# Kernel tuning notes

Hardware: AMD Instinct MI355X
Metric: run time of the kernel (lower is better)

The kernel has to match this reference:

```python
import jax, jax.numpy as jnp
import numpy as np

ETA = 1e-5
MIN_SIGMA = 1e-6

def setup_inputs() -> dict:
    key = jax.random.key(0)
    k1, k2, k3, k4 = jax.random.split(key, 4)
    B, N0, N1, D = 32, 1024, 1024, 128
    xt = jax.random.normal(k1, (B, D), dtype=jnp.float32)
    t = jax.random.uniform(k2, (B,), dtype=jnp.float32)
    x0_ref = jax.random.normal(k3, (N0, D), dtype=jnp.float32)
    x1_ref = jax.random.normal(k4, (N1, D), dtype=jnp.float32)
    sigma_w = jnp.zeros((1,), dtype=jnp.float32)  # learned scalar of the sigma_model
    return {"xt": xt, "t": t, "x0_ref": x0_ref, "x1_ref": x1_ref, "sigma_w": sigma_w}


def reference(xt, t, x0_ref, x1_ref, sigma_w):
    # Equivalent to ExplicitFlowMatcher.compute_explicit_flow_vcond (implementation='vcond',
    # use_full_gaussian_prefactor=True). The chunked online-softmax loop computes exactly a
    # softmax over all (N0,N1) pairs; here we express it with GEMMs instead of materializing
    # the [B,N0,N1,D] conditional-flow tensor (v_cond is affine in x0, x1, xt so the weighted
    # sum decomposes into matmuls).
    B, D = xt.shape
    Df = jnp.asarray(D, xt.dtype)

    # pairwise squared distances ||x1_j - x0_i||^2 via norms + GEMM  -> [N0,N1]
    x0n = jnp.sum(x0_ref * x0_ref, axis=-1)            # [N0]
    x1n = jnp.sum(x1_ref * x1_ref, axis=-1)            # [N1]
    dot01 = x0_ref @ x1_ref.T                          # [N0,N1]
    dist01 = x0n[:, None] + x1n[None, :] - 2.0 * dot01  # [N0,N1]

    # sigma_model: softplus(w)*||x1-x0||/sqrt(D) + min_sigma, then bridge scale in t
    sigma_space = jax.nn.softplus(sigma_w[0]) * jnp.sqrt(jnp.maximum(dist01, 0.0) / Df) + MIN_SIGMA
    bridge = jnp.sqrt((t + ETA) * (1.0 - t + ETA))     # [B]
    sigma_t = sigma_space[None, :, :] * bridge[:, None, None]  # [B,N0,N1]

    # ||xt_b - mu_t(i,j)||^2 with mu_t = (1-t)x0 + t x1, expanded into GEMM terms
    tb = t[:, None, None]
    omt = 1.0 - tb
    xtn = jnp.sum(xt * xt, axis=-1)                    # [B]
    xt_x0 = xt @ x0_ref.T                              # [B,N0]
    xt_x1 = xt @ x1_ref.T                              # [B,N1]
    mu_norm2 = (omt * omt) * x0n[None, :, None] + (tb * tb) * x1n[None, None, :] \
               + (2.0 * tb * omt) * dot01[None, :, :]
    xt_mu = omt * xt_x0[:, :, None] + tb * xt_x1[:, None, :]
    dist2 = xtn[:, None, None] - 2.0 * xt_mu + mu_norm2  # [B,N0,N1]

    # Gaussian log-weight with full prefactor
    logw = -dist2 / (2.0 * sigma_t * sigma_t) - Df * jnp.log(sigma_t)  # [B,N0,N1]

    # stable softmax over the (N0,N1) pairs (== the online max/den/num recursion)
    m = jnp.max(logw, axis=(1, 2), keepdims=True)
    w = jnp.exp(logw - m)                               # [B,N0,N1]
    den = jnp.sum(w, axis=(1, 2))                       # [B]

    # v_cond = x1 - x0 + c_t*(xt - mu_t) = c_t*xt + a*x0 + b*x1 (affine in x0,x1)
    c_t = (1.0 - 2.0 * t) / (2.0 * (t + ETA) * (1.0 - t + ETA))  # [B]
    a = -1.0 - c_t * (1.0 - t)
    b = 1.0 - c_t * t
    wx0 = jnp.einsum('bij,id->bd', w, x0_ref)
    wx1 = jnp.einsum('bij,jd->bd', w, x1_ref)

    den_c = jnp.maximum(den, 1e-12)[:, None]
    num = c_t[:, None] * xt * den[:, None] + a[:, None] * wx0 + b[:, None] * wx1
    return num / den_c
```

## Files before the change

kernel.cpp:

```cpp
#include <hip/hip_runtime.h>
#include <math.h>

#define ETA 1e-5f
#define MIN_SIGMA 1e-6f

constexpr int NN = 1024;
constexpr int ND = 128;

constexpr size_t OFF_MAXKEY = 0;
constexpr size_t OFF_DEN    = 32;
constexpr size_t OFF_RW     = 64;
constexpr size_t OFF_CW     = OFF_RW + 32 * 1024;
constexpr size_t OFF_X0N    = OFF_CW + 32 * 1024;
constexpr size_t OFF_X1N    = OFF_X0N + 1024;
constexpr size_t OFF_AP     = OFF_X1N + 1024;
constexpr size_t OFF_BP     = OFF_AP + 32 * 1024;
constexpr size_t OFF_C2     = OFF_BP + 32 * 1024;
constexpr size_t OFF_DOT    = ((OFF_C2 + 32 + 63) / 64) * 64;

__device__ __forceinline__ unsigned fkey(float x) {
  unsigned u = __float_as_uint(x);
  return (u & 0x80000000u) ? ~u : (u | 0x80000000u);
}
__device__ __forceinline__ float funkey(unsigned u) {
  return (u & 0x80000000u) ? __uint_as_float(u & 0x7fffffffu)
                           : __uint_as_float(~u);
}

__global__ __launch_bounds__(256) void k_ab(const float* __restrict__ xt,
                                            const float* __restrict__ tarr,
                                            const float* __restrict__ x0,
                                            const float* __restrict__ x1,
                                            float* __restrict__ ws) {
  __shared__ __align__(16) float xts[ND];
  int b = blockIdx.x >> 2, q = blockIdx.x & 3;
  int tid = threadIdx.x;
  if (tid < ND) xts[tid] = xt[(size_t)b * ND + tid];
  __syncthreads();

  float tb = tarr[b];
  float omt = 1.f - tb;
  float ib2 = 1.f / ((tb + ETA) * (1.f - tb + ETA));

  float xtn = 0.f;
#pragma unroll
  for (int k4 = 0; k4 < ND / 4; k4++) {
    float4 xv = *(const float4*)&xts[k4 * 4];
    xtn += xv.x * xv.x + xv.y * xv.y + xv.z * xv.z + xv.w * xv.w;
  }

  int i = q * 256 + tid;
  float acc0 = 0.f, acc1 = 0.f, n0 = 0.f, n1 = 0.f;
#pragma unroll 8
  for (int k4 = 0; k4 < ND / 4; k4++) {
    float4 xv = *(const float4*)&xts[k4 * 4];
    float4 a = *(const float4*)(x0 + (size_t)i * ND + k4 * 4);
    float4 c = *(const float4*)(x1 + (size_t)i * ND + k4 * 4);
    acc0 += xv.x * a.x + xv.y * a.y + xv.z * a.z + xv.w * a.w;
    acc1 += xv.x * c.x + xv.y * c.y + xv.z * c.z + xv.w * c.w;
    n0 += a.x * a.x + a.y * a.y + a.z * a.z + a.w * a.w;
    n1 += c.x * c.x + c.y * c.y + c.z * c.z + c.w * c.w;
  }
  ws[OFF_AP + (size_t)b * NN + i] =
      fmaf(omt * omt, n0, fmaf(-2.f * omt, acc0, xtn)) * ib2;
  ws[OFF_BP + (size_t)b * NN + i] =
      fmaf(tb * tb, n1, -2.f * tb * acc1) * ib2;
  if (b == 0) {
    ws[OFF_X0N + i] = n0;
    ws[OFF_X1N + i] = n1;
  }
  if (q == 0 && tid == 0) ws[OFF_C2 + b] = 2.f * tb * omt * ib2;
}

__global__ __launch_bounds__(256) void k1(const float* __restrict__ x0,
                                          const float* __restrict__ x1,
                                          const float* __restrict__ sigw,
                                          float* __restrict__ ws) {
  __shared__ __align__(16) float As[32][36];
  __shared__ __align__(16) float Bs[32][36];
  __shared__ __align__(16) float4 QPRS[32][32];
  __shared__ float ApT[32][33], BpT[32][33];
  __shared__ float x0nS[32], x1nS[32];
  __shared__ unsigned mS[32];

  int tid = threadIdx.x;
  int tx = tid & 15, ty = tid >> 4;
  int i0 = blockIdx.y * 32, j0 = blockIdx.x * 32;

  {
    const float* Ap = ws + OFF_AP;
    const float* Bp = ws + OFF_BP;
#pragma unroll
    for (int rep = 0; rep < 4; rep++) {
      int idx = rep * 256 + tid;
      int bb = idx >> 5, ii = idx & 31;
      ApT[ii][bb] = Ap[(size_t)bb * NN + i0 + ii];
      BpT[ii][bb] = Bp[(size_t)bb * NN + j0 + ii];
    }
    if (tid < 32) {
      x0nS[tid] = ws[OFF_X0N + i0 + tid];
      x1nS[tid] = ws[OFF_X1N + j0 + tid];
      mS[tid] = 0u;
    }
  }

  float c00 = 0.f, c01 = 0.f, c10 = 0.f, c11 = 0.f;
  int srow = tid >> 3, sk4 = tid & 7;
  for (int kc = 0; kc < 4; kc++) {
    __syncthreads();
    float4 a = *(const float4*)(x0 + (size_t)(i0 + srow) * ND + kc * 32 + sk4 * 4);
    float4 bb = *(const float4*)(x1 + (size_t)(j0 + srow) * ND + kc * 32 + sk4 * 4);
    As[sk4 * 4 + 0][srow] = a.x;
    As[sk4 * 4 + 1][srow] = a.y;
    As[sk4 * 4 + 2][srow] = a.z;
    As[sk4 * 4 + 3][srow] = a.w;
    Bs[sk4 * 4 + 0][srow] = bb.x;
    Bs[sk4 * 4 + 1][srow] = bb.y;
    Bs[sk4 * 4 + 2][srow] = bb.z;
    Bs[sk4 * 4 + 3][srow] = bb.w;
    __syncthreads();
#pragma unroll
    for (int k = 0; k < 32; k++) {
      float2 av = *(const float2*)&As[k][ty * 2];
      float2 bv = *(const float2*)&Bs[k][tx * 2];
      c00 = fmaf(av.x, bv.x, c00);
      c01 = fmaf(av.x, bv.y, c01);
      c10 = fmaf(av.y, bv.x, c10);
      c11 = fmaf(av.y, bv.y, c11);
    }
  }

  float* dot = ws + OFF_DOT;
  *(float2*)&dot[(size_t)(i0 + ty * 2 + 0) * NN + j0 + tx * 2] = make_float2(c00, c01);
  *(float2*)&dot[(size_t)(i0 + ty * 2 + 1) * NN + j0 + tx * 2] = make_float2(c10, c11);

  float swv = sigw[0];
  float sp = (swv > 20.f) ? swv : log1pf(__expf(swv));
  float dotv[2][2] = {{c00, c01}, {c10, c11}};
#pragma unroll
  for (int r = 0; r < 2; r++) {
#pragma unroll
    for (int c = 0; c < 2; c++) {
      float d01 = x0nS[ty * 2 + r] + x1nS[tx * 2 + c] - 2.f * dotv[r][c];
      float ss = fmaf(sp, sqrtf(fmaxf(d01, 0.f) * (1.f / 128.f)), MIN_SIGMA);
      float Q = -0.72134752044f / (ss * ss);
      float R = -128.f * __log2f(ss);
      QPRS[ty * 2 + r][tx * 2 + c] = make_float4(Q, dotv[r][c] * Q, R, 0.f);
    }
  }
  __syncthreads();

  int b = tid & 31, rep = tid >> 5;
  float c2b = ws[OFF_C2 + b];
  float bpreg[32];
#pragma unroll
  for (int j = 0; j < 32; j++) bpreg[j] = BpT[j][b];
  float m = -3.4e38f;
#pragma unroll
  for (int r = 0; r < 4; r++) {
    int i = rep * 4 + r;
    float ap = ApT[i][b];
#pragma unroll
    for (int j = 0; j < 32; j++) {
      float4 q4 = QPRS[i][j];
      float core = fmaf(ap + bpreg[j], q4.x, fmaf(c2b, q4.y, q4.z));
      m = fmaxf(m, core);
    }
  }
  atomicMax(&mS[b], fkey(m));
  __syncthreads();
  if (tid < 32) atomicMax((unsigned*)ws + OFF_MAXKEY + tid, mS[tid]);
}

__global__ __launch_bounds__(256) void k2(const float* __restrict__ sigw,
                                          float* __restrict__ ws) {
  __shared__ __align__(16) float4 QPRS[32][32];
  __shared__ float ApT[32][33], BpT[32][33];
  __shared__ float colS[32][33], rowS[32][33];
  __shared__ float x0nS[32], x1nS[32];
  __shared__ float denS[32];

  int tid = threadIdx.x;
  int tx = tid & 15, ty = tid >> 4;
  int i0 = blockIdx.y * 32, j0 = blockIdx.x * 32;

  {
    const float* Ap = ws + OFF_AP;
    const float* Bp = ws + OFF_BP;
#pragma unroll
    for (int rep = 0; rep < 4; rep++) {
      int idx = rep * 256 + tid;
      int bb = idx >> 5, ii = idx & 31;
      ApT[ii][bb] = Ap[(size_t)bb * NN + i0 + ii];
      BpT[ii][bb] = Bp[(size_t)bb * NN + j0 + ii];
      colS[ii][bb] = 0.f;
    }
    if (tid < 32) {
      x0nS[tid] = ws[OFF_X0N + i0 + tid];
      x1nS[tid] = ws[OFF_X1N + j0 + tid];
      denS[tid] = 0.f;
    }
  }

  const float* dot = ws + OFF_DOT;
  float2 dv0 = *(const float2*)&dot[(size_t)(i0 + ty * 2 + 0) * NN + j0 + tx * 2];
  float2 dv1 = *(const float2*)&dot[(size_t)(i0 + ty * 2 + 1) * NN + j0 + tx * 2];
  float dotv[2][2] = {{dv0.x, dv0.y}, {dv1.x, dv1.y}};
  float swv = sigw[0];
  float sp = (swv > 20.f) ? swv : log1pf(__expf(swv));

  __syncthreads();

#pragma unroll
  for (int r = 0; r < 2; r++) {
#pragma unroll
    for (int c = 0; c < 2; c++) {
      float d01 = x0nS[ty * 2 + r] + x1nS[tx * 2 + c] - 2.f * dotv[r][c];
      float ss = fmaf(sp, sqrtf(fmaxf(d01, 0.f) * (1.f / 128.f)), MIN_SIGMA);
      float Q = -0.72134752044f / (ss * ss);
      float R = -128.f * __log2f(ss);
      QPRS[ty * 2 + r][tx * 2 + c] = make_float4(Q, dotv[r][c] * Q, R, 0.f);
    }
  }
  __syncthreads();

  int b = tid & 31, rep = tid >> 5;
  float c2b = ws[OFF_C2 + b];
  float m2 = funkey(((const unsigned*)ws)[OFF_MAXKEY + b]);
  float bpreg[32];
#pragma unroll
  for (int j = 0; j < 32; j++) bpreg[j] = BpT[j][b];
  float colreg[32];
#pragma unroll
  for (int j = 0; j < 32; j++) colreg[j] = 0.f;
  float dreg = 0.f;
#pragma unroll
  for (int r = 0; r < 4; r++) {
    int i = rep * 4 + r;
    float ap = ApT[i][b];
    float rs = 0.f;
#pragma unroll
    for (int j = 0; j < 32; j++) {
      float4 q4 = QPRS[i][j];
      float core = fmaf(ap + bpreg[j], q4.x, fmaf(c2b, q4.y, q4.z));
      float w = exp2f(core - m2);
      rs += w;
      colreg[j] += w;
    }
    rowS[i][b] = rs;
    dreg += rs;
  }
#pragma unroll
  for (int j = 0; j < 32; j++) atomicAdd(&colS[j][b], colreg[j]);
  atomicAdd(&denS[b], dreg);
  __syncthreads();

  float* rw = ws + OFF_RW;
  float* cw = ws + OFF_CW;
#pragma unroll
  for (int k = 0; k < 4; k++) {
    int idx = k * 256 + tid;
    int bb = idx >> 5, ii = idx & 31;
    atomicAdd(&rw[(size_t)bb * NN + i0 + ii], rowS[ii][bb]);
    atomicAdd(&cw[(size_t)bb * NN + j0 + ii], colS[ii][bb]);
  }
  if (tid < 32) atomicAdd(ws + OFF_DEN + tid, denS[tid]);
}

__global__ __launch_bounds__(256) void k3(const float* __restrict__ xt,
                                          const float* __restrict__ tarr,
                                          const float* __restrict__ x0,
                                          const float* __restrict__ x1,
                                          const float* __restrict__ ws,
                                          float* __restrict__ out) {
  int b = blockIdx.x >> 2, dq = blockIdx.x & 3;
  int tid = threadIdx.x;
  int d = dq * 32 + (tid & 31);
  int h = tid >> 5;
  const float* rw = ws + OFF_RW + (size_t)b * NN;
  const float* cw = ws + OFF_CW + (size_t)b * NN;
  float a0 = 0.f, a1 = 0.f;
  int ibeg = h * 128;
#pragma unroll 4
  for (int k = 0; k < 128; k++) {
    int i = ibeg + k;
    a0 = fmaf(rw[i], x0[(size_t)i * ND + d], a0);
    a1 = fmaf(cw[i], x1[(size_t)i * ND + d], a1);
  }
  __shared__ float s0[8][32], s1[8][32];
  s0[h][tid & 31] = a0;
  s1[h][tid & 31] = a1;
  __syncthreads();
  if (tid < 32) {
    float A0 = 0.f, A1 = 0.f;
#pragma unroll
    for (int hh = 0; hh < 8; hh++) {
      A0 += s0[hh][tid];
      A1 += s1[hh][tid];
    }
    float tb = tarr[b];
    float den = ws[OFF_DEN + b];
    float ct = (1.f - 2.f * tb) / (2.f * (tb + ETA) * (1.f - tb + ETA));
    float av = -1.f - ct * (1.f - tb);
    float bv = 1.f - ct * tb;
    float den_c = fmaxf(den, 1e-12f);
    out[(size_t)b * ND + d] =
        (ct * xt[(size_t)b * ND + d] * den + av * A0 + bv * A1) / den_c;
  }
}

extern "C" void kernel_launch(void* const* d_in, const int* in_sizes, int n_in,
                              void* d_out, int out_size, void* d_ws, size_t ws_size,
                              hipStream_t stream) {
  const float* xt = (const float*)d_in[0];
  const float* t = (const float*)d_in[1];
  const float* x0 = (const float*)d_in[2];
  const float* x1 = (const float*)d_in[3];
  const float* sw = (const float*)d_in[4];
  float* out = (float*)d_out;
  float* ws = (float*)d_ws;

  hipMemsetAsync(ws, 0, OFF_X0N * sizeof(float), stream);

  k_ab<<<128, 256, 0, stream>>>(xt, t, x0, x1, ws);
  k1<<<dim3(32, 32), 256, 0, stream>>>(x0, x1, sw, ws);
  k2<<<dim3(32, 32), 256, 0, stream>>>(sw, ws);
  k3<<<128, 256, 0, stream>>>(xt, t, x0, x1, ws, out);
}
```

Before: 168.6 us.

## Fuse max and weight passes into one tile kernel with per-tile partial rescale

Replaces the separate max kernel and weight-sum kernel (which recomputed or stored the dot tile) with a single kernel. For each tile it computes the local max, tile-local exp sums for rows and columns, and the per-tile max. A new reduction kernel finds the global max and rescales the partial row and column sums with exp2(mloc - mg), then accumulates den. This removes one pass over the N0xN1 work and the dot-matrix round trip, at the cost of a much larger workspace of partials (32x32x1024 floats each for rows and columns). The new path only runs when the workspace is large enough; otherwise it falls back to the old kernels.

```diff
diff --git a/kernel.cpp b/kernel.cpp
--- a/kernel.cpp
+++ b/kernel.cpp
@@ -16,7 +16,12 @@
 constexpr size_t OFF_AP     = OFF_X1N + 1024;
 constexpr size_t OFF_BP     = OFF_AP + 32 * 1024;
 constexpr size_t OFF_C2     = OFF_BP + 32 * 1024;
-constexpr size_t OFF_DOT    = ((OFF_C2 + 32 + 63) / 64) * 64;
+constexpr size_t OFF_RWP    = ((OFF_C2 + 32 + 63) / 64) * 64;
+constexpr size_t OFF_DOT    = OFF_RWP;
+constexpr size_t OFF_CWP    = OFF_RWP + 32 * 32 * 1024;
+constexpr size_t OFF_MLOC   = OFF_CWP + 32 * 32 * 1024;
+constexpr size_t WS_NEED_FUSED = OFF_MLOC + 32 * 32 * 32;
+constexpr size_t WS_NEED_FALLBACK = OFF_DOT + 1024 * 1024;
 
 __device__ __forceinline__ unsigned fkey(float x) {
   unsigned u = __float_as_uint(x);
@@ -70,6 +75,183 @@
     ws[OFF_X1N + i] = n1;
   }
   if (q == 0 && tid == 0) ws[OFF_C2 + b] = 2.f * tb * omt * ib2;
+}
+
+__global__ __launch_bounds__(256) void kF(const float* __restrict__ x0,
+                                          const float* __restrict__ x1,
+                                          const float* __restrict__ sigw,
+                                          float* __restrict__ ws) {
+  __shared__ __align__(16) float gemmbuf[2304];
+  __shared__ __align__(16) float4 QPRS[32][32];
+  __shared__ float ApT[32][33], BpT[32][33];
+  __shared__ float x0nS[32], x1nS[32];
+  __shared__ unsigned mS[32];
+
+  float (*As)[36] = (float(*)[36])&gemmbuf[0];
+  float (*Bs)[36] = (float(*)[36])&gemmbuf[1152];
+  float (*rowS)[33] = (float(*)[33])&gemmbuf[0];
+  float (*colS)[33] = (float(*)[33])&gemmbuf[1056];
+
+  int tid = threadIdx.x;
+  int tx = tid & 15, ty = tid >> 4;
+  int jb = blockIdx.x, ib = blockIdx.y;
+  int i0 = ib * 32, j0 = jb * 32;
+
+  {
+    const float* Ap = ws + OFF_AP;
+    const float* Bp = ws + OFF_BP;
+#pragma unroll
+    for (int rep = 0; rep < 4; rep++) {
+      int idx = rep * 256 + tid;
+      int bb = idx >> 5, ii = idx & 31;
+      ApT[ii][bb] = Ap[(size_t)bb * NN + i0 + ii];
+      BpT[ii][bb] = Bp[(size_t)bb * NN + j0 + ii];
+    }
+    if (tid < 32) {
+      x0nS[tid] = ws[OFF_X0N + i0 + tid];
+      x1nS[tid] = ws[OFF_X1N + j0 + tid];
+      mS[tid] = 0u;
+    }
+  }
+
+  float c00 = 0.f, c01 = 0.f, c10 = 0.f, c11 = 0.f;
+  int srow = tid >> 3, sk4 = tid & 7;
+  for (int kc = 0; kc < 4; kc++) {
+    __syncthreads();
+    float4 a = *(const float4*)(x0 + (size_t)(i0 + srow) * ND + kc * 32 + sk4 * 4);
+    float4 bb = *(const float4*)(x1 + (size_t)(j0 + srow) * ND + kc * 32 + sk4 * 4);
+    As[sk4 * 4 + 0][srow] = a.x;
+    As[sk4 * 4 + 1][srow] = a.y;
+    As[sk4 * 4 + 2][srow] = a.z;
+    As[sk4 * 4 + 3][srow] = a.w;
+    Bs[sk4 * 4 + 0][srow] = bb.x;
+    Bs[sk4 * 4 + 1][srow] = bb.y;
+    Bs[sk4 * 4 + 2][srow] = bb.z;
+    Bs[sk4 * 4 + 3][srow] = bb.w;
+    __syncthreads();
+#pragma unroll
+    for (int k = 0; k < 32; k++) {
+      float2 av = *(const float2*)&As[k][ty * 2];
+      float2 bv = *(const float2*)&Bs[k][tx * 2];
+      c00 = fmaf(av.x, bv.x, c00);
+      c01 = fmaf(av.x, bv.y, c01);
+      c10 = fmaf(av.y, bv.x, c10);
+      c11 = fmaf(av.y, bv.y, c11);
+    }
+  }
+
+  float swv = sigw[0];
+  float sp = (swv > 20.f) ? swv : log1pf(__expf(swv));
+  float dotv[2][2] = {{c00, c01}, {c10, c11}};
+#pragma unroll
+  for (int r = 0; r < 2; r++) {
+#pragma unroll
+    for (int c = 0; c < 2; c++) {
+      float d01 = x0nS[ty * 2 + r] + x1nS[tx * 2 + c] - 2.f * dotv[r][c];
+      float ss = fmaf(sp, sqrtf(fmaxf(d01, 0.f) * (1.f / 128.f)), MIN_SIGMA);
+      float Q = -0.72134752044f / (ss * ss);
+      float R = -128.f * __log2f(ss);
+      QPRS[ty * 2 + r][tx * 2 + c] = make_float4(Q, dotv[r][c] * Q, R, 0.f);
+    }
+  }
+  __syncthreads();
+
+  for (int idx = tid; idx < 1056; idx += 256) ((float*)colS)[idx] = 0.f;
+  int b = tid & 31, rep = tid >> 5;
+  float c2b = ws[OFF_C2 + b];
+  float bpreg[32];
+#pragma unroll
+  for (int j = 0; j < 32; j++) bpreg[j] = BpT[j][b];
+  float m = -3.4e38f;
+#pragma unroll
+  for (int r = 0; r < 4; r++) {
+    int i = rep * 4 + r;
+    float ap = ApT[i][b];
+#pragma unroll
+    for (int j = 0; j < 32; j++) {
+      float4 q4 = QPRS[i][j];
+      float core = fmaf(ap + bpreg[j], q4.x, fmaf(c2b, q4.y, q4.z));
+      m = fmaxf(m, core);
+    }
+  }
+  atomicMax(&mS[b], fkey(m));
+  __syncthreads();
+
+  float m2 = funkey(mS[b]);
+  float colreg[32];
+#pragma unroll
+  for (int j = 0; j < 32; j++) colreg[j] = 0.f;
+#pragma unroll
+  for (int r = 0; r < 4; r++) {
+    int i = rep * 4 + r;
+    float ap = ApT[i][b];
+    float rs = 0.f;
+#pragma unroll
+    for (int j = 0; j < 32; j++) {
+      float4 q4 = QPRS[i][j];
+      float core = fmaf(ap + bpreg[j], q4.x, fmaf(c2b, q4.y, q4.z));
+      float w = exp2f(core - m2);
+      rs += w;
+      colreg[j] += w;
+    }
+    rowS[i][b] = rs;
+  }
+#pragma unroll
+  for (int j = 0; j < 32; j++) atomicAdd(&colS[j][b], colreg[j]);
+  __syncthreads();
+
+  float* rwp = ws + OFF_RWP + (size_t)jb * (32 * 1024);
+  float* cwp = ws + OFF_CWP + (size_t)ib * (32 * 1024);
+#pragma unroll
+  for (int k = 0; k < 4; k++) {
+    int idx = k * 256 + tid;
+    int bb = idx >> 5, ii = idx & 31;
+    rwp[(size_t)bb * NN + i0 + ii] = rowS[ii][bb];
+    cwp[(size_t)bb * NN + j0 + ii] = colS[ii][bb];
+  }
+  if (tid < 32) ws[OFF_MLOC + ((size_t)ib * 32 + jb) * 32 + tid] = funkey(mS[tid]);
+}
+
+__global__ __launch_bounds__(256) void kR(float* __restrict__ ws) {
+  __shared__ float red[256];
+  int b = blockIdx.x >> 2, quarter = blockIdx.x & 3;
+  int tid = threadIdx.x;
+
+  const float* ml = ws + OFF_MLOC + b;
+  float mx = -3.4e38f;
+#pragma unroll
+  for (int k = 0; k < 4; k++) mx = fmaxf(mx, ml[(size_t)(k * 256 + tid) * 32]);
+  red[tid] = mx;
+  __syncthreads();
+  for (int s = 128; s > 0; s >>= 1) {
+    if (tid < s) red[tid] = fmaxf(red[tid], red[tid + s]);
+    __syncthreads();
+  }
+  float mg = red[0];
+  __syncthreads();
+
+  int i = quarter * 256 + tid;
+  int tb = i >> 5;
+  const float* rwp = ws + OFF_RWP + (size_t)b * NN + i;
+  const float* cwp = ws + OFF_CWP + (size_t)b * NN + i;
+  const float* mlI = ws + OFF_MLOC + (size_t)tb * 1024 + b;
+  const float* mlJ = ws + OFF_MLOC + (size_t)tb * 32 + b;
+  float s0 = 0.f, s1 = 0.f;
+#pragma unroll 8
+  for (int p = 0; p < 32; p++) {
+    s0 = fmaf(exp2f(mlI[(size_t)p * 32] - mg), rwp[(size_t)p * 32 * 1024], s0);
+    s1 = fmaf(exp2f(mlJ[(size_t)p * 1024] - mg), cwp[(size_t)p * 32 * 1024], s1);
+  }
+  ws[OFF_RW + (size_t)b * NN + i] = s0;
+  ws[OFF_CW + (size_t)b * NN + i] = s1;
+
+  red[tid] = s0;
+  __syncthreads();
+  for (int s = 128; s > 0; s >>= 1) {
+    if (tid < s) red[tid] += red[tid + s];
+    __syncthreads();
+  }
+  if (tid == 0) atomicAdd(ws + OFF_DEN + b, red[0]);
 }
 
 __global__ __launch_bounds__(256) void k1(const float* __restrict__ x0,
@@ -320,10 +502,18 @@
   float* out = (float*)d_out;
   float* ws = (float*)d_ws;
 
-  hipMemsetAsync(ws, 0, OFF_X0N * sizeof(float), stream);
-
-  k_ab<<<128, 256, 0, stream>>>(xt, t, x0, x1, ws);
-  k1<<<dim3(32, 32), 256, 0, stream>>>(x0, x1, sw, ws);
-  k2<<<dim3(32, 32), 256, 0, stream>>>(sw, ws);
+  bool fused = ws_size >= WS_NEED_FUSED * sizeof(float);
+
+  if (fused) {
+    hipMemsetAsync(ws, 0, 64 * sizeof(float), stream);
+    k_ab<<<128, 256, 0, stream>>>(xt, t, x0, x1, ws);
+    kF<<<dim3(32, 32), 256, 0, stream>>>(x0, x1, sw, ws);
+    kR<<<128, 256, 0, stream>>>(ws);
+  } else {
+    hipMemsetAsync(ws, 0, OFF_X0N * sizeof(float), stream);
+    k_ab<<<128, 256, 0, stream>>>(xt, t, x0, x1, ws);
+    k1<<<dim3(32, 32), 256, 0, stream>>>(x0, x1, sw, ws);
+    k2<<<dim3(32, 32), 256, 0, stream>>>(sw, ws);
+  }
   k3<<<128, 256, 0, stream>>>(xt, t, x0, x1, ws, out);
 }
```

After: 164.3 us. 2.5% less time.
